# Optimization experiments

Hardware: AMD Instinct MI355X
Metric: run time of the kernel (lower is better)

The kernel has to match this reference:

```python
import jax, jax.numpy as jnp
import numpy as np

C = 64
K = 3  # kernel_size
B, H, W = 8, 128, 128


def conv2d(x, w, b, pad, groups=1):
    y = jax.lax.conv_general_dilated(
        x, w, window_strides=(1, 1), padding=[(pad, pad), (pad, pad)],
        feature_group_count=groups, dimension_numbers=('NCHW', 'OIHW', 'NCHW'))
    return y + b[None, :, None, None]


def setup_inputs() -> dict:
    key = jax.random.key(0)
    ks = jax.random.split(key, 11)
    s3 = 1.0 / np.sqrt(C * 9)  # kaiming-ish scale for 3x3 convs
    inp = {
        'x':  jax.random.normal(ks[0], (B, C, H, W), jnp.float32),
        'w0': jax.random.normal(ks[1], (C, C, 3, 3), jnp.float32) * s3,
        'b0': jax.random.normal(ks[2], (C,), jnp.float32) * 0.01,
        'w1': jax.random.normal(ks[3], (C, 1, 3, 3), jnp.float32) * (1.0 / 3.0),  # depthwise
        'b1': jax.random.normal(ks[4], (C,), jnp.float32) * 0.01,
        'w2': jax.random.normal(ks[5], (1, 1, K), jnp.float32) * (1.0 / np.sqrt(K)),  # conv1d over channel axis
        'b2': jax.random.normal(ks[6], (1,), jnp.float32) * 0.01,
        'w3': jax.random.normal(ks[7], (C * K * K, C, 1, 1), jnp.float32) * (1.0 / np.sqrt(C)),  # 1x1 -> dynamic filters
        'b3': jax.random.normal(ks[8], (C * K * K,), jnp.float32) * 0.01,
        'wf': jax.random.normal(ks[9], (C, C, 3, 3), jnp.float32) * s3,
        'bf': jax.random.normal(ks[10], (C,), jnp.float32) * 0.01,
    }
    return inp


def reference(x, w0, b0, w1, b1, w2, b2, w3, b3, wf, bf):
    b, c, h, w = x.shape
    pre = x
    # conv0: dense 3x3
    x0 = conv2d(x, w0, b0, pad=1)
    # conv1: depthwise 3x3
    x1 = conv2d(x0, w1, b1, pad=1, groups=c)
    # ECA-style channel attention: global avg pool -> conv1d over channel dim
    m = jnp.mean(x0, axis=(2, 3))  # [b, c]
    x2 = jax.lax.conv_general_dilated(
        m[:, None, :], w2, window_strides=(1,), padding=[(K // 2, K // 2)],
        dimension_numbers=('NCH', 'OIH', 'NCH')) + b2[None, :, None]  # [b, 1, c]
    out = x1 + x2[:, 0, :, None, None]  # broadcast [b,c,1,1] over h,w
    # conv3: 1x1 producing per-pixel dynamic filters [b, c*9, h, w]
    fil = jnp.einsum('oc,bchw->bohw', w3[:, :, 0, 0], out) + b3[None, :, None, None]
    filter_x = fil.reshape(b, c, K * K, h, w)
    # unfold(x0): 3x3 patches, channel-major then row-major kernel positions
    xp = jnp.pad(x0, ((0, 0), (0, 0), (1, 1), (1, 1)))
    unfold_x = jnp.stack(
        [xp[:, :, i:i + h, j:j + w] for i in range(3) for j in range(3)], axis=2)  # [b,c,9,h,w]
    out = jnp.sum(unfold_x * filter_x, axis=2)  # per-pixel dynamic conv
    out = jnp.where(out >= 0, out, 0.2 * out)  # LeakyReLU(0.2)
    out = conv2d(out, wf, bf, pad=1) + pre
    return out
```

## Files before the change

### kernel.cpp

```cpp
#include <hip/hip_runtime.h>

#define BB 8
#define C 64
#define HH 128
#define WW 128
#define HW (HH*WW)

#define TS 72
#define NPX 324

typedef __attribute__((ext_vector_type(8))) short short8;
typedef __attribute__((ext_vector_type(4))) unsigned short us4;
typedef __attribute__((ext_vector_type(4))) float f32x4;

__device__ inline unsigned short f2bf(float f) {
    union { float f; unsigned u; } v; v.f = f;
    unsigned r = v.u + 0x7fff + ((v.u >> 16) & 1);
    return (unsigned short)(r >> 16);
}
__device__ inline float bf2f(unsigned short h) {
    union { unsigned u; float f; } v; v.u = ((unsigned)h) << 16;
    return v.f;
}

__global__ __launch_bounds__(256) void prep_kernel(
    const float* __restrict__ w0, const float* __restrict__ wf,
    const float* __restrict__ w3, const float* __restrict__ b3,
    unsigned short* __restrict__ wb0, unsigned short* __restrict__ wbf,
    unsigned short* __restrict__ wb3, float* __restrict__ b3r,
    float* __restrict__ m)
{
    const int t = blockIdx.x * 256 + threadIdx.x;
    for (int i = t; i < C*C*9; i += 32*256) {
        int p = i % 9; int rest = i / 9; int ci = rest % C; int oc = rest / C;
        wb0[(p*C + oc)*C + ci] = f2bf(w0[i]);
        wbf[(p*C + oc)*C + ci] = f2bf(wf[i]);
    }
    for (int i = t; i < 9*C*C; i += 32*256) {
        int j = i >> 12, oc = (i >> 6) & 63, k = i & 63;
        wb3[i] = f2bf(w3[(oc*9 + j)*C + k]);
    }
    for (int i = t; i < 9*C; i += 32*256) {
        int j = i >> 6, oc = i & 63;
        b3r[i] = b3[oc*9 + j];
    }
    for (int i = t; i < BB*C; i += 32*256) m[i] = 0.f;
}

template<bool FIRST>
__global__ __launch_bounds__(256, 3) void conv_mfma_kernel(
    const void* __restrict__ in,
    const unsigned short* __restrict__ wb,
    const float* __restrict__ bias,
    const float* __restrict__ res,
    void* __restrict__ outp,
    float* __restrict__ m)
{
    __shared__ __align__(16) unsigned short tile[NPX*TS];
    __shared__ __align__(16) float sred[4][4][16];
    const int b  = blockIdx.z;
    const int h0 = blockIdx.y * 16;
    const int w0 = blockIdx.x * 16;
    const int t  = threadIdx.x;

    {
        const int pxi = t & 31, g = t >> 5;
        for (int px = pxi; px < NPX; px += 32) {
            int th = px / 18, tw = px - th*18;
            int gh = h0 + th - 1, gw = w0 + tw - 1;
            short8 v = {0,0,0,0,0,0,0,0};
            if ((unsigned)gh < HH && (unsigned)gw < WW) {
                if (FIRST) {
                    const float* sp = (const float*)in
                        + ((size_t)(b*C + g*8)*HW + gh*WW + gw);
#pragma unroll
                    for (int k = 0; k < 8; ++k) v[k] = (short)f2bf(sp[k*HW]);
                } else {
                    v = *(const short8*)((const unsigned short*)in
                        + ((size_t)(b*HW) + gh*WW + gw)*C + g*8);
                }
            }
            *(short8*)&tile[px*TS + g*8] = v;
        }
    }
    __syncthreads();

    const int wid = t >> 6, ln = t & 63;
    const int l15 = ln & 15, q = ln >> 4;

    f32x4 acc[4][4];
#pragma unroll
    for (int mg = 0; mg < 4; ++mg)
#pragma unroll
        for (int nt = 0; nt < 4; ++nt) acc[mg][nt] = (f32x4){0.f,0.f,0.f,0.f};

#pragma unroll 1
    for (int p = 0; p < 9; ++p) {
        const int dh = p / 3, dw = p - dh*3;
#pragma unroll
        for (int ks = 0; ks < 2; ++ks) {
            short8 bfrag[4];
#pragma unroll
            for (int nt = 0; nt < 4; ++nt)
                bfrag[nt] = *(const short8*)&wb[((size_t)(p*C) + nt*16 + l15)*C + ks*32 + q*8];
            short8 afrag[4];
#pragma unroll
            for (int mg = 0; mg < 4; ++mg) {
                const int r = wid*4 + mg;
                afrag[mg] = *(const short8*)&tile[((r+dh)*18 + l15 + dw)*TS + ks*32 + q*8];
            }
#pragma unroll
            for (int mg = 0; mg < 4; ++mg)
#pragma unroll
                for (int nt = 0; nt < 4; ++nt)
                    acc[mg][nt] = __builtin_amdgcn_mfma_f32_16x16x32_bf16(
                        afrag[mg], bfrag[nt], acc[mg][nt], 0, 0, 0);
        }
    }

    if (FIRST) {
        unsigned short* x0o = (unsigned short*)outp;
#pragma unroll
        for (int nt = 0; nt < 4; ++nt) {
            const int oc = nt*16 + l15;
            const float bv = bias[oc];
            float s = 0.f;
#pragma unroll
            for (int mg = 0; mg < 4; ++mg) {
                const int hh = h0 + wid*4 + mg;
#pragma unroll
                for (int reg = 0; reg < 4; ++reg) {
                    const int wwp = w0 + q*4 + reg;
                    const unsigned short sv = f2bf(acc[mg][nt][reg] + bv);
                    x0o[((size_t)(b*HW) + hh*WW + wwp)*C + oc] = sv;
                    s += bf2f(sv);
                }
            }
            s += __shfl_xor(s, 16);
            s += __shfl_xor(s, 32);
            if (q == 0) sred[wid][nt][l15] = s;
        }
        __syncthreads();
        if (t < 64) {
            float s = sred[0][t >> 4][t & 15] + sred[1][t >> 4][t & 15]
                    + sred[2][t >> 4][t & 15] + sred[3][t >> 4][t & 15];
            atomicAdd(&m[b*C + t], s * (1.f/(float)HW));
        }
    } else {
        float* outg = (float*)outp;
#pragma unroll
        for (int mg = 0; mg < 4; ++mg) {
            const int hh = h0 + wid*4 + mg;
#pragma unroll
            for (int nt = 0; nt < 4; ++nt) {
                const int oc = nt*16 + l15;
                const float bv = bias[oc];
                const size_t base = (size_t)(b*C + oc)*HW + hh*WW + w0 + q*4;
                const float4 rv = *(const float4*)&res[base];
                float4 ov;
                ov.x = acc[mg][nt][0] + bv + rv.x;
                ov.y = acc[mg][nt][1] + bv + rv.y;
                ov.z = acc[mg][nt][2] + bv + rv.z;
                ov.w = acc[mg][nt][3] + bv + rv.w;
                *(float4*)&outg[base] = ov;
            }
        }
    }
}

__global__ __launch_bounds__(256) void fused_kernel(
    const unsigned short* __restrict__ x0,
    const float* __restrict__ w1, const float* __restrict__ b1,
    const float* __restrict__ w2, const float* __restrict__ b2,
    const unsigned short* __restrict__ wb3,
    const float* __restrict__ b3r,
    const float* __restrict__ m,
    unsigned short* __restrict__ y)
{
    __shared__ __align__(16) unsigned short tile[NPX*TS];
    __shared__ __align__(16) unsigned short alds[256*64];
    __shared__ __align__(16) float att[64];
    const int b  = blockIdx.z;
    const int h0 = blockIdx.y * 16;
    const int w0 = blockIdx.x * 16;
    const int t  = threadIdx.x;

    if (t < 64) {
        const float mc = m[b*C + t];
        const float mp = (t > 0)  ? m[b*C + t - 1] : 0.f;
        const float mn = (t < 63) ? m[b*C + t + 1] : 0.f;
        att[t] = b1[t] + fmaf(w2[0], mp, fmaf(w2[1], mc, fmaf(w2[2], mn, b2[0])));
    }
    {
        const int pxi = t & 31, g = t >> 5;
        for (int px = pxi; px < NPX; px += 32) {
            int th = px / 18, tw = px - th*18;
            int gh = h0 + th - 1, gw = w0 + tw - 1;
            short8 v = {0,0,0,0,0,0,0,0};
            if ((unsigned)gh < HH && (unsigned)gw < WW)
                v = *(const short8*)&x0[((size_t)(b*HW) + gh*WW + gw)*C + g*8];
            *(short8*)&tile[px*TS + g*8] = v;
        }
    }
    __syncthreads();

    const int r = t >> 4, cc = t & 15;
    const unsigned short* tbase = tile + (r*18 + cc)*TS;

    float outv[64];
#pragma unroll
    for (int g = 0; g < 8; ++g) {
        float dw8[8];
#pragma unroll
        for (int k = 0; k < 8; ++k) dw8[k] = 0.f;
#pragma unroll
        for (int j = 0; j < 9; ++j) {
            short8 v = *(const short8*)&tbase[((j/3)*18 + (j%3))*TS + g*8];
#pragma unroll
            for (int k = 0; k < 8; ++k)
                dw8[k] = fmaf(w1[(g*8+k)*9 + j], bf2f((unsigned short)v[k]), dw8[k]);
        }
#pragma unroll
        for (int k = 0; k < 8; ++k) {
            const int c = g*8 + k;
            outv[c] = dw8[k] + att[c];
        }
    }

    {
        const int sw = t & 7;
#pragma unroll
        for (int g = 0; g < 8; ++g) {
            short8 v;
#pragma unroll
            for (int k = 0; k < 8; ++k) v[k] = (short)f2bf(outv[g*8 + k]);
            *(short8*)&alds[t*64 + ((g ^ sw) * 8)] = v;
        }
    }
    __syncthreads();

    const int wid = t >> 6, ln = t & 63;
    const int l15 = ln & 15, q = ln >> 4;

    short8 afrag[4][2];
#pragma unroll
    for (int mg = 0; mg < 4; ++mg) {
        const int px = (wid*4 + mg)*16 + l15;
        const int sw = px & 7;
#pragma unroll
        for (int ks = 0; ks < 2; ++ks)
            afrag[mg][ks] = *(const short8*)&alds[px*64 + (((ks*4 + q) ^ sw) * 8)];
    }

    f32x4 y_acc[4][4];
#pragma unroll
    for (int mg = 0; mg < 4; ++mg)
#pragma unroll
        for (int nt = 0; nt < 4; ++nt) y_acc[mg][nt] = (f32x4){0.f,0.f,0.f,0.f};

#pragma unroll 1
    for (int j = 0; j < 9; ++j) {
        const int dh = j / 3, dw = j - dh*3;
#pragma unroll
        for (int ntoc = 0; ntoc < 4; ++ntoc) {
            const short8 bf0 = *(const short8*)&wb3[((size_t)(j*64 + ntoc*16 + l15))*64 + q*8];
            const short8 bf1 = *(const short8*)&wb3[((size_t)(j*64 + ntoc*16 + l15))*64 + 32 + q*8];
            const f32x4 b3v4 = *(const f32x4*)&b3r[j*64 + ntoc*16 + q*4];
#pragma unroll
            for (int mg = 0; mg < 4; ++mg) {
                f32x4 a = b3v4;
                a = __builtin_amdgcn_mfma_f32_16x16x32_bf16(bf0, afrag[mg][0], a, 0, 0, 0);
                a = __builtin_amdgcn_mfma_f32_16x16x32_bf16(bf1, afrag[mg][1], a, 0, 0, 0);
                const int rr = wid*4 + mg;
                const us4 pv = *(const us4*)
                    &tile[((rr+dh)*18 + l15 + dw)*TS + ntoc*16 + q*4];
#pragma unroll
                for (int reg = 0; reg < 4; ++reg)
                    y_acc[mg][ntoc][reg] = fmaf(a[reg], bf2f(pv[reg]), y_acc[mg][ntoc][reg]);
            }
        }
    }

    __syncthreads();
    unsigned short* ybuf = alds;
#pragma unroll
    for (int mg = 0; mg < 4; ++mg) {
        const int rr = wid*4 + mg;
        const int px = rr*16 + l15;
        const int swy = (px & 7) << 1;
#pragma unroll
        for (int ntoc = 0; ntoc < 4; ++ntoc) {
            us4 ov;
#pragma unroll
            for (int reg = 0; reg < 4; ++reg) {
                float v = y_acc[mg][ntoc][reg];
                v = (v >= 0.f) ? v : 0.2f * v;
                ov[reg] = f2bf(v);
            }
            const int slot = (ntoc*4 + q) ^ swy;
            *(us4*)&ybuf[px*64 + slot*4] = ov;
        }
    }
    __syncthreads();
    for (int id = t; id < 2048; id += 256) {
        int px = id >> 3, g = id & 7;
        const int swy = (px & 7) << 1;
        short8 v = *(const short8*)&ybuf[px*64 + ((2*g) ^ swy)*4];
        int rr = px >> 4, cw = px & 15;
        *(short8*)&y[((size_t)(b*HW) + (h0+rr)*WW + (w0+cw))*C + g*8] = v;
    }
}

extern "C" void kernel_launch(void* const* d_in, const int* in_sizes, int n_in,
                              void* d_out, int out_size, void* d_ws, size_t ws_size,
                              hipStream_t stream) {
    const float* x  = (const float*)d_in[0];
    const float* w0 = (const float*)d_in[1];
    const float* b0 = (const float*)d_in[2];
    const float* w1 = (const float*)d_in[3];
    const float* b1 = (const float*)d_in[4];
    const float* w2 = (const float*)d_in[5];
    const float* b2 = (const float*)d_in[6];
    const float* w3 = (const float*)d_in[7];
    const float* b3 = (const float*)d_in[8];
    const float* wf = (const float*)d_in[9];
    const float* bf = (const float*)d_in[10];
    float* out = (float*)d_out;

    unsigned short* x0  = (unsigned short*)d_ws;
    unsigned short* y   = x0 + (size_t)BB*HW*C;
    float*          m   = (float*)(y + (size_t)BB*HW*C);
    unsigned short* wb0 = (unsigned short*)(m + BB*C);
    unsigned short* wbf = wb0 + 9*C*C;
    unsigned short* wb3 = wbf + 9*C*C;
    float*          b3r = (float*)(wb3 + 9*C*C);

    prep_kernel<<<32, 256, 0, stream>>>(w0, wf, w3, b3, wb0, wbf, wb3, b3r, m);
    conv_mfma_kernel<true><<<dim3(8,8,8), 256, 0, stream>>>(x, wb0, b0, nullptr, x0, m);
    fused_kernel<<<dim3(8,8,8), 256, 0, stream>>>(x0, w1, b1, w2, b2, wb3, b3r, m, y);
    conv_mfma_kernel<false><<<dim3(8,8,8), 256, 0, stream>>>(y, wbf, bf, x, out, nullptr);
}
```

Before: 210.0 us.

## Merge four kernel launches into one cooperative persistent kernel with grid syncs

Replaces the prep, first conv, fused dynamic-filter and final conv launches with a single cooperative kernel that separates the phases with grid.sync(). The aim is to remove per-launch overhead and the gaps between kernels. If the cooperative launch fails, the original four-kernel sequence runs instead. The trade-offs are grid-wide barrier cost and a requirement that all 512 blocks be co-resident. The merged kernel also needs LDS for the largest phase in every phase, which may limit occupancy, and the launch bounds were relaxed to 2 blocks per unit.

```diff
diff --git a/kernel.cpp b/kernel.cpp
--- a/kernel.cpp
+++ b/kernel.cpp
@@ -1,4 +1,7 @@
 #include <hip/hip_runtime.h>
+#include <hip/hip_cooperative_groups.h>
+
+namespace cg = cooperative_groups;
 
 #define BB 8
 #define C 64
@@ -23,51 +26,22 @@
     return v.f;
 }
 
-__global__ __launch_bounds__(256) void prep_kernel(
-    const float* __restrict__ w0, const float* __restrict__ wf,
-    const float* __restrict__ w3, const float* __restrict__ b3,
-    unsigned short* __restrict__ wb0, unsigned short* __restrict__ wbf,
-    unsigned short* __restrict__ wb3, float* __restrict__ b3r,
-    float* __restrict__ m)
-{
-    const int t = blockIdx.x * 256 + threadIdx.x;
-    for (int i = t; i < C*C*9; i += 32*256) {
-        int p = i % 9; int rest = i / 9; int ci = rest % C; int oc = rest / C;
-        wb0[(p*C + oc)*C + ci] = f2bf(w0[i]);
-        wbf[(p*C + oc)*C + ci] = f2bf(wf[i]);
-    }
-    for (int i = t; i < 9*C*C; i += 32*256) {
-        int j = i >> 12, oc = (i >> 6) & 63, k = i & 63;
-        wb3[i] = f2bf(w3[(oc*9 + j)*C + k]);
-    }
-    for (int i = t; i < 9*C; i += 32*256) {
-        int j = i >> 6, oc = i & 63;
-        b3r[i] = b3[oc*9 + j];
-    }
-    for (int i = t; i < BB*C; i += 32*256) m[i] = 0.f;
-}
-
 template<bool FIRST>
-__global__ __launch_bounds__(256, 3) void conv_mfma_kernel(
+__device__ __forceinline__ void conv_phase(
     const void* __restrict__ in,
     const unsigned short* __restrict__ wb,
     const float* __restrict__ bias,
     const float* __restrict__ res,
     void* __restrict__ outp,
-    float* __restrict__ m)
-{
-    __shared__ __align__(16) unsigned short tile[NPX*TS];
-    __shared__ __align__(16) float sred[4][4][16];
-    const int b  = blockIdx.z;
-    const int h0 = blockIdx.y * 16;
-    const int w0 = blockIdx.x * 16;
-    const int t  = threadIdx.x;
-
+    float* __restrict__ m,
+    unsigned short* tile, float* sredf,
+    const int b, const int h0, const int wc0, const int t)
+{
     {
         const int pxi = t & 31, g = t >> 5;
         for (int px = pxi; px < NPX; px += 32) {
             int th = px / 18, tw = px - th*18;
-            int gh = h0 + th - 1, gw = w0 + tw - 1;
+            int gh = h0 + th - 1, gw = wc0 + tw - 1;
             short8 v = {0,0,0,0,0,0,0,0};
             if ((unsigned)gh < HH && (unsigned)gw < WW) {
                 if (FIRST) {
@@ -130,7 +104,7 @@
                 const int hh = h0 + wid*4 + mg;
 #pragma unroll
                 for (int reg = 0; reg < 4; ++reg) {
-                    const int wwp = w0 + q*4 + reg;
+                    const int wwp = wc0 + q*4 + reg;
                     const unsigned short sv = f2bf(acc[mg][nt][reg] + bv);
                     x0o[((size_t)(b*HW) + hh*WW + wwp)*C + oc] = sv;
                     s += bf2f(sv);
@@ -138,14 +112,16 @@
             }
             s += __shfl_xor(s, 16);
             s += __shfl_xor(s, 32);
-            if (q == 0) sred[wid][nt][l15] = s;
+            if (q == 0) sredf[(wid*4 + nt)*16 + l15] = s;
         }
         __syncthreads();
         if (t < 64) {
-            float s = sred[0][t >> 4][t & 15] + sred[1][t >> 4][t & 15]
-                    + sred[2][t >> 4][t & 15] + sred[3][t >> 4][t & 15];
+            const int nt2 = t >> 4, l2 = t & 15;
+            float s = sredf[(0*4 + nt2)*16 + l2] + sredf[(1*4 + nt2)*16 + l2]
+                    + sredf[(2*4 + nt2)*16 + l2] + sredf[(3*4 + nt2)*16 + l2];
             atomicAdd(&m[b*C + t], s * (1.f/(float)HW));
         }
+        __syncthreads();
     } else {
         float* outg = (float*)outp;
 #pragma unroll
@@ -155,7 +131,7 @@
             for (int nt = 0; nt < 4; ++nt) {
                 const int oc = nt*16 + l15;
                 const float bv = bias[oc];
-                const size_t base = (size_t)(b*C + oc)*HW + hh*WW + w0 + q*4;
+                const size_t base = (size_t)(b*C + oc)*HW + hh*WW + wc0 + q*4;
                 const float4 rv = *(const float4*)&res[base];
                 float4 ov;
                 ov.x = acc[mg][nt][0] + bv + rv.x;
@@ -166,6 +142,228 @@
             }
         }
     }
+}
+
+__device__ __forceinline__ void fused_phase(
+    const unsigned short* __restrict__ x0,
+    const float* __restrict__ w1, const float* __restrict__ b1,
+    const float* __restrict__ w2, const float* __restrict__ b2,
+    const unsigned short* __restrict__ wb3,
+    const float* __restrict__ b3r,
+    const float* __restrict__ m,
+    unsigned short* __restrict__ y,
+    unsigned short* tile, unsigned short* alds, float* att,
+    const int b, const int h0, const int wc0, const int t)
+{
+    if (t < 64) {
+        const float mc = m[b*C + t];
+        const float mp = (t > 0)  ? m[b*C + t - 1] : 0.f;
+        const float mn = (t < 63) ? m[b*C + t + 1] : 0.f;
+        att[t] = b1[t] + fmaf(w2[0], mp, fmaf(w2[1], mc, fmaf(w2[2], mn, b2[0])));
+    }
+    {
+        const int pxi = t & 31, g = t >> 5;
+        for (int px = pxi; px < NPX; px += 32) {
+            int th = px / 18, tw = px - th*18;
+            int gh = h0 + th - 1, gw = wc0 + tw - 1;
+            short8 v = {0,0,0,0,0,0,0,0};
+            if ((unsigned)gh < HH && (unsigned)gw < WW)
+                v = *(const short8*)&x0[((size_t)(b*HW) + gh*WW + gw)*C + g*8];
+            *(short8*)&tile[px*TS + g*8] = v;
+        }
+    }
+    __syncthreads();
+
+    const int r = t >> 4, cc = t & 15;
+    const unsigned short* tbase = tile + (r*18 + cc)*TS;
+
+    float outv[64];
+#pragma unroll
+    for (int g = 0; g < 8; ++g) {
+        float dw8[8];
+#pragma unroll
+        for (int k = 0; k < 8; ++k) dw8[k] = 0.f;
+#pragma unroll
+        for (int j = 0; j < 9; ++j) {
+            short8 v = *(const short8*)&tbase[((j/3)*18 + (j%3))*TS + g*8];
+#pragma unroll
+            for (int k = 0; k < 8; ++k)
+                dw8[k] = fmaf(w1[(g*8+k)*9 + j], bf2f((unsigned short)v[k]), dw8[k]);
+        }
+#pragma unroll
+        for (int k = 0; k < 8; ++k) {
+            const int c = g*8 + k;
+            outv[c] = dw8[k] + att[c];
+        }
+    }
+
+    {
+        const int sw = t & 7;
+#pragma unroll
+        for (int g = 0; g < 8; ++g) {
+            short8 v;
+#pragma unroll
+            for (int k = 0; k < 8; ++k) v[k] = (short)f2bf(outv[g*8 + k]);
+            *(short8*)&alds[t*64 + ((g ^ sw) * 8)] = v;
+        }
+    }
+    __syncthreads();
+
+    const int wid = t >> 6, ln = t & 63;
+    const int l15 = ln & 15, q = ln >> 4;
+
+    short8 afrag[4][2];
+#pragma unroll
+    for (int mg = 0; mg < 4; ++mg) {
+        const int px = (wid*4 + mg)*16 + l15;
+        const int sw = px & 7;
+#pragma unroll
+        for (int ks = 0; ks < 2; ++ks)
+            afrag[mg][ks] = *(const short8*)&alds[px*64 + (((ks*4 + q) ^ sw) * 8)];
+    }
+
+    f32x4 y_acc[4][4];
+#pragma unroll
+    for (int mg = 0; mg < 4; ++mg)
+#pragma unroll
+        for (int nt = 0; nt < 4; ++nt) y_acc[mg][nt] = (f32x4){0.f,0.f,0.f,0.f};
+
+#pragma unroll 1
+    for (int j = 0; j < 9; ++j) {
+        const int dh = j / 3, dw = j - dh*3;
+#pragma unroll
+        for (int ntoc = 0; ntoc < 4; ++ntoc) {
+            const short8 bf0 = *(const short8*)&wb3[((size_t)(j*64 + ntoc*16 + l15))*64 + q*8];
+            const short8 bf1 = *(const short8*)&wb3[((size_t)(j*64 + ntoc*16 + l15))*64 + 32 + q*8];
+            const f32x4 b3v4 = *(const f32x4*)&b3r[j*64 + ntoc*16 + q*4];
+#pragma unroll
+            for (int mg = 0; mg < 4; ++mg) {
+                f32x4 a = b3v4;
+                a = __builtin_amdgcn_mfma_f32_16x16x32_bf16(bf0, afrag[mg][0], a, 0, 0, 0);
+                a = __builtin_amdgcn_mfma_f32_16x16x32_bf16(bf1, afrag[mg][1], a, 0, 0, 0);
+                const int rr = wid*4 + mg;
+                const us4 pv = *(const us4*)
+                    &tile[((rr+dh)*18 + l15 + dw)*TS + ntoc*16 + q*4];
+#pragma unroll
+                for (int reg = 0; reg < 4; ++reg)
+                    y_acc[mg][ntoc][reg] = fmaf(a[reg], bf2f(pv[reg]), y_acc[mg][ntoc][reg]);
+            }
+        }
+    }
+
+    __syncthreads();
+    unsigned short* ybuf = alds;
+#pragma unroll
+    for (int mg = 0; mg < 4; ++mg) {
+        const int rr = wid*4 + mg;
+        const int px = rr*16 + l15;
+        const int swy = (px & 7) << 1;
+#pragma unroll
+        for (int ntoc = 0; ntoc < 4; ++ntoc) {
+            us4 ov;
+#pragma unroll
+            for (int reg = 0; reg < 4; ++reg) {
+                float v = y_acc[mg][ntoc][reg];
+                v = (v >= 0.f) ? v : 0.2f * v;
+                ov[reg] = f2bf(v);
+            }
+            const int slot = (ntoc*4 + q) ^ swy;
+            *(us4*)&ybuf[px*64 + slot*4] = ov;
+        }
+    }
+    __syncthreads();
+    for (int id = t; id < 2048; id += 256) {
+        int px = id >> 3, g = id & 7;
+        const int swy = (px & 7) << 1;
+        short8 v = *(const short8*)&ybuf[px*64 + ((2*g) ^ swy)*4];
+        int rr = px >> 4, cw = px & 15;
+        *(short8*)&y[((size_t)(b*HW) + (h0+rr)*WW + (wc0+cw))*C + g*8] = v;
+    }
+}
+
+__global__ __launch_bounds__(256, 2) void mega_kernel(
+    const float* __restrict__ x,
+    const float* __restrict__ w0, const float* __restrict__ b0,
+    const float* __restrict__ w1, const float* __restrict__ b1,
+    const float* __restrict__ w2, const float* __restrict__ b2,
+    const float* __restrict__ w3, const float* __restrict__ b3,
+    const float* __restrict__ wf, const float* __restrict__ bf,
+    float* __restrict__ out,
+    unsigned short* __restrict__ x0, unsigned short* __restrict__ y,
+    float* __restrict__ m,
+    unsigned short* __restrict__ wb0, unsigned short* __restrict__ wbf,
+    unsigned short* __restrict__ wb3, float* __restrict__ b3r)
+{
+    __shared__ __align__(16) unsigned short tile[NPX*TS];
+    __shared__ __align__(16) unsigned short alds[256*64];
+    __shared__ __align__(16) float att[64];
+
+    cg::grid_group grid = cg::this_grid();
+
+    const int b   = blockIdx.z;
+    const int h0  = blockIdx.y * 16;
+    const int wc0 = blockIdx.x * 16;
+    const int t   = threadIdx.x;
+    const int bid = (blockIdx.z * 8 + blockIdx.y) * 8 + blockIdx.x;
+    const int gt  = bid * 256 + t;
+
+    if (gt < C*C*9) {
+        int p = gt % 9; int rest = gt / 9; int ci = rest % C; int oc = rest / C;
+        wb0[(p*C + oc)*C + ci] = f2bf(w0[gt]);
+        wbf[(p*C + oc)*C + ci] = f2bf(wf[gt]);
+        int j = gt >> 12, oc2 = (gt >> 6) & 63, k = gt & 63;
+        wb3[gt] = f2bf(w3[(oc2*9 + j)*C + k]);
+    }
+    if (gt < 9*C) { int j = gt >> 6, oc = gt & 63; b3r[gt] = b3[oc*9 + j]; }
+    if (gt < BB*C) m[gt] = 0.f;
+    grid.sync();
+
+    conv_phase<true>(x, wb0, b0, nullptr, x0, m, tile, (float*)alds, b, h0, wc0, t);
+    grid.sync();
+
+    fused_phase(x0, w1, b1, w2, b2, wb3, b3r, m, y, tile, alds, att, b, h0, wc0, t);
+    grid.sync();
+
+    conv_phase<false>(y, wbf, bf, x, out, nullptr, tile, (float*)alds, b, h0, wc0, t);
+}
+
+__global__ __launch_bounds__(256) void prep_kernel(
+    const float* __restrict__ w0, const float* __restrict__ wf,
+    const float* __restrict__ w3, const float* __restrict__ b3,
+    unsigned short* __restrict__ wb0, unsigned short* __restrict__ wbf,
+    unsigned short* __restrict__ wb3, float* __restrict__ b3r,
+    float* __restrict__ m)
+{
+    const int t = blockIdx.x * 256 + threadIdx.x;
+    for (int i = t; i < C*C*9; i += 32*256) {
+        int p = i % 9; int rest = i / 9; int ci = rest % C; int oc = rest / C;
+        wb0[(p*C + oc)*C + ci] = f2bf(w0[i]);
+        wbf[(p*C + oc)*C + ci] = f2bf(wf[i]);
+    }
+    for (int i = t; i < 9*C*C; i += 32*256) {
+        int j = i >> 12, oc = (i >> 6) & 63, k = i & 63;
+        wb3[i] = f2bf(w3[(oc*9 + j)*C + k]);
+    }
+    for (int i = t; i < 9*C; i += 32*256) {
+        int j = i >> 6, oc = i & 63;
+        b3r[i] = b3[oc*9 + j];
+    }
+    for (int i = t; i < BB*C; i += 32*256) m[i] = 0.f;
+}
+
+template<bool FIRST>
+__global__ __launch_bounds__(256) void conv_mfma_kernel(
+    const void* __restrict__ in,
+    const unsigned short* __restrict__ wb,
+    const float* __restrict__ bias,
+    const float* __restrict__ res,
+    void* __restrict__ outp,
+    float* __restrict__ m)
+{
+    __shared__ __align__(16) unsigned short tile[NPX*TS];
+    __shared__ __align__(16) float sred[4*4*16];
+    conv_phase<FIRST>(in, wb, bias, res, outp, m, tile, sred,
+                      blockIdx.z, blockIdx.y*16, blockIdx.x*16, threadIdx.x);
 }
 
 __global__ __launch_bounds__(256) void fused_kernel(
@@ -180,135 +378,8 @@
     __shared__ __align__(16) unsigned short tile[NPX*TS];
     __shared__ __align__(16) unsigned short alds[256*64];
     __shared__ __align__(16) float att[64];
-    const int b  = blockIdx.z;
-    const int h0 = blockIdx.y * 16;
-    const int w0 = blockIdx.x * 16;
-    const int t  = threadIdx.x;
-
-    if (t < 64) {
-        const float mc = m[b*C + t];
-        const float mp = (t > 0)  ? m[b*C + t - 1] : 0.f;
-        const float mn = (t < 63) ? m[b*C + t + 1] : 0.f;
-        att[t] = b1[t] + fmaf(w2[0], mp, fmaf(w2[1], mc, fmaf(w2[2], mn, b2[0])));
-    }
-    {
-        const int pxi = t & 31, g = t >> 5;
-        for (int px = pxi; px < NPX; px += 32) {
-            int th = px / 18, tw = px - th*18;
-            int gh = h0 + th - 1, gw = w0 + tw - 1;
-            short8 v = {0,0,0,0,0,0,0,0};
-            if ((unsigned)gh < HH && (unsigned)gw < WW)
-                v = *(const short8*)&x0[((size_t)(b*HW) + gh*WW + gw)*C + g*8];
-            *(short8*)&tile[px*TS + g*8] = v;
-        }
-    }
-    __syncthreads();
-
-    const int r = t >> 4, cc = t & 15;
-    const unsigned short* tbase = tile + (r*18 + cc)*TS;
-
-    float outv[64];
-#pragma unroll
-    for (int g = 0; g < 8; ++g) {
-        float dw8[8];
-#pragma unroll
-        for (int k = 0; k < 8; ++k) dw8[k] = 0.f;
-#pragma unroll
-        for (int j = 0; j < 9; ++j) {
-            short8 v = *(const short8*)&tbase[((j/3)*18 + (j%3))*TS + g*8];
-#pragma unroll
-            for (int k = 0; k < 8; ++k)
-                dw8[k] = fmaf(w1[(g*8+k)*9 + j], bf2f((unsigned short)v[k]), dw8[k]);
-        }
-#pragma unroll
-        for (int k = 0; k < 8; ++k) {
-            const int c = g*8 + k;
-            outv[c] = dw8[k] + att[c];
-        }
-    }
-
-    {
-        const int sw = t & 7;
-#pragma unroll
-        for (int g = 0; g < 8; ++g) {
-            short8 v;
-#pragma unroll
-            for (int k = 0; k < 8; ++k) v[k] = (short)f2bf(outv[g*8 + k]);
-            *(short8*)&alds[t*64 + ((g ^ sw) * 8)] = v;
-        }
-    }
-    __syncthreads();
-
-    const int wid = t >> 6, ln = t & 63;
-    const int l15 = ln & 15, q = ln >> 4;
-
-    short8 afrag[4][2];
-#pragma unroll
-    for (int mg = 0; mg < 4; ++mg) {
-        const int px = (wid*4 + mg)*16 + l15;
-        const int sw = px & 7;
-#pragma unroll
-        for (int ks = 0; ks < 2; ++ks)
-            afrag[mg][ks] = *(const short8*)&alds[px*64 + (((ks*4 + q) ^ sw) * 8)];
-    }
-
-    f32x4 y_acc[4][4];
-#pragma unroll
-    for (int mg = 0; mg < 4; ++mg)
-#pragma unroll
-        for (int nt = 0; nt < 4; ++nt) y_acc[mg][nt] = (f32x4){0.f,0.f,0.f,0.f};
-
-#pragma unroll 1
-    for (int j = 0; j < 9; ++j) {
-        const int dh = j / 3, dw = j - dh*3;
-#pragma unroll
-        for (int ntoc = 0; ntoc < 4; ++ntoc) {
-            const short8 bf0 = *(const short8*)&wb3[((size_t)(j*64 + ntoc*16 + l15))*64 + q*8];
-            const short8 bf1 = *(const short8*)&wb3[((size_t)(j*64 + ntoc*16 + l15))*64 + 32 + q*8];
-            const f32x4 b3v4 = *(const f32x4*)&b3r[j*64 + ntoc*16 + q*4];
-#pragma unroll
-            for (int mg = 0; mg < 4; ++mg) {
-                f32x4 a = b3v4;
-                a = __builtin_amdgcn_mfma_f32_16x16x32_bf16(bf0, afrag[mg][0], a, 0, 0, 0);
-                a = __builtin_amdgcn_mfma_f32_16x16x32_bf16(bf1, afrag[mg][1], a, 0, 0, 0);
-                const int rr = wid*4 + mg;
-                const us4 pv = *(const us4*)
-                    &tile[((rr+dh)*18 + l15 + dw)*TS + ntoc*16 + q*4];
-#pragma unroll
-                for (int reg = 0; reg < 4; ++reg)
-                    y_acc[mg][ntoc][reg] = fmaf(a[reg], bf2f(pv[reg]), y_acc[mg][ntoc][reg]);
-            }
-        }
-    }
-
-    __syncthreads();
-    unsigned short* ybuf = alds;
-#pragma unroll
-    for (int mg = 0; mg < 4; ++mg) {
-        const int rr = wid*4 + mg;
-        const int px = rr*16 + l15;
-        const int swy = (px & 7) << 1;
-#pragma unroll
-        for (int ntoc = 0; ntoc < 4; ++ntoc) {
-            us4 ov;
-#pragma unroll
-            for (int reg = 0; reg < 4; ++reg) {
-                float v = y_acc[mg][ntoc][reg];
-                v = (v >= 0.f) ? v : 0.2f * v;
-                ov[reg] = f2bf(v);
-            }
-            const int slot = (ntoc*4 + q) ^ swy;
-            *(us4*)&ybuf[px*64 + slot*4] = ov;
-        }
-    }
-    __syncthreads();
-    for (int id = t; id < 2048; id += 256) {
-        int px = id >> 3, g = id & 7;
-        const int swy = (px & 7) << 1;
-        short8 v = *(const short8*)&ybuf[px*64 + ((2*g) ^ swy)*4];
-        int rr = px >> 4, cw = px & 15;
-        *(short8*)&y[((size_t)(b*HW) + (h0+rr)*WW + (w0+cw))*C + g*8] = v;
-    }
+    fused_phase(x0, w1, b1, w2, b2, wb3, b3r, m, y, tile, alds, att,
+                blockIdx.z, blockIdx.y*16, blockIdx.x*16, threadIdx.x);
 }
 
 extern "C" void kernel_launch(void* const* d_in, const int* in_sizes, int n_in,
@@ -335,8 +406,19 @@
     unsigned short* wb3 = wbf + 9*C*C;
     float*          b3r = (float*)(wb3 + 9*C*C);
 
-    prep_kernel<<<32, 256, 0, stream>>>(w0, wf, w3, b3, wb0, wbf, wb3, b3r, m);
-    conv_mfma_kernel<true><<<dim3(8,8,8), 256, 0, stream>>>(x, wb0, b0, nullptr, x0, m);
-    fused_kernel<<<dim3(8,8,8), 256, 0, stream>>>(x0, w1, b1, w2, b2, wb3, b3r, m, y);
-    conv_mfma_kernel<false><<<dim3(8,8,8), 256, 0, stream>>>(y, wbf, bf, x, out, nullptr);
-}
+    void* args[] = {
+        (void*)&x,  (void*)&w0, (void*)&b0, (void*)&w1, (void*)&b1,
+        (void*)&w2, (void*)&b2, (void*)&w3, (void*)&b3, (void*)&wf,
+        (void*)&bf, (void*)&out, (void*)&x0, (void*)&y,  (void*)&m,
+        (void*)&wb0, (void*)&wbf, (void*)&wb3, (void*)&b3r
+    };
+    hipError_t e = hipLaunchCooperativeKernel(
+        mega_kernel, dim3(8,8,8), dim3(256,1,1), args, 0u, stream);
+
+    if (e != hipSuccess) {
+        prep_kernel<<<32, 256, 0, stream>>>(w0, wf, w3, b3, wb0, wbf, wb3, b3r, m);
+        conv_mfma_kernel<true><<<dim3(8,8,8), 256, 0, stream>>>(x, wb0, b0, nullptr, x0, m);
+        fused_kernel<<<dim3(8,8,8), 256, 0, stream>>>(x0, w1, b1, w2, b2, wb3, b3r, m, y);
+        conv_mfma_kernel<false><<<dim3(8,8,8), 256, 0, stream>>>(y, wbf, bf, x, out, nullptr);
+    }
+}
```

Result: slower. 372.9 us (+77.6%).
